# Optimization experiments

Hardware: AMD Instinct MI355X
Metric: run time of the kernel (lower is better)

The kernel has to match this reference:

```python
import jax, jax.numpy as jnp
import numpy as np

B, N, T, CIN, COUT, K, DIL = 8, 207, 12, 64, 64, 3, 1


def setup_inputs() -> dict:
    key = jax.random.key(0)
    ks = jax.random.split(key, 13)
    s = 0.05
    return {
        "X": jax.random.normal(ks[0], (B, N, T, CIN), jnp.float32),
        "wA": jax.random.normal(ks[1], (COUT, CIN, 1, K), jnp.float32) * s,
        "bA": jax.random.normal(ks[2], (COUT,), jnp.float32) * s,
        "wB": jax.random.normal(ks[3], (COUT, CIN, 1, K), jnp.float32) * s,
        "bB": jax.random.normal(ks[4], (COUT,), jnp.float32) * s,
        "wq": jax.random.normal(ks[5], (COUT // 8, COUT), jnp.float32) * s,
        "bq": jax.random.normal(ks[6], (COUT // 8,), jnp.float32) * s,
        "wk": jax.random.normal(ks[7], (COUT // 8, COUT), jnp.float32) * s,
        "bk": jax.random.normal(ks[8], (COUT // 8,), jnp.float32) * s,
        "wv": jax.random.normal(ks[9], (COUT, COUT), jnp.float32) * s,
        "bv": jax.random.normal(ks[10], (COUT,), jnp.float32) * s,
        "gamma": jax.random.normal(ks[11], (1,), jnp.float32) * 0.1,
    }


def reference(X, wA, bA, wB, bB, wq, bq, wk, bk, wv, bv, gamma):
    # X: [B, N, T, C] -> [B, C, N, T]
    x = jnp.transpose(X, (0, 3, 1, 2))
    k_size = wA.shape[-1]
    pad = (k_size - 1) * DIL  # causal left pad == pad-both + drop-right in torch code

    def causal_conv(w, b):
        y = jax.lax.conv_general_dilated(
            x, w, window_strides=(1, 1),
            padding=((0, 0), (pad, 0)),
            rhs_dilation=(1, DIL),
            dimension_numbers=("NCHW", "OIHW", "NCHW"))
        return y + b[None, :, None, None]

    A = causal_conv(wA, bA)
    Bg = causal_conv(wB, bB)
    h = A * jax.nn.sigmoid(Bg)  # [B, C, N, T]

    b_, c, w_, h_ = h.shape
    L = w_ * h_
    h2 = h.reshape(b_, c, L)  # [B, C, L]
    q = jnp.einsum("oc,bcl->bol", wq, h2) + bq[None, :, None]  # [B, C/8, L]
    kk = jnp.einsum("oc,bcl->bol", wk, h2) + bk[None, :, None]
    v = jnp.einsum("oc,bcl->bol", wv, h2) + bv[None, :, None]   # [B, C, L]

    energy = jnp.einsum("bql,bqm->blm", q, kk)  # [B, L, L]
    attn = jax.nn.softmax(energy, axis=-1)
    out = jnp.einsum("bcm,blm->bcl", v, attn).reshape(b_, c, w_, h_)
    out = gamma[0] * out + h
    return jnp.transpose(out, (0, 2, 3, 1))  # [B, N, T, C]
```

## Files before the change

### kernel.cpp

```cpp
#include <hip/hip_runtime.h>
#include <hip/hip_bf16.h>

#define Bn 8
#define Nn 207
#define Tn 12
#define Cn 64
#define Ln (Nn*Tn)
#define LP 2496
#define NT 39
#define NB 104

typedef unsigned int u32;
typedef unsigned short u16;
typedef _Float16 f16;
typedef __fp16 h16;
typedef __attribute__((ext_vector_type(2))) __fp16 h16x2;
typedef __attribute__((ext_vector_type(4))) __fp16 h16x4;
typedef __attribute__((ext_vector_type(4))) float floatx4;

#define LOG2E 1.44269504088896f

__device__ __forceinline__ u16 f2h(float f) { f16 h = (f16)f; return *(u16*)&h; }
__device__ __forceinline__ float h2f_lo(u32 u) { u16 x = (u16)u;        f16 h = *(f16*)&x; return (float)h; }
__device__ __forceinline__ float h2f_hi(u32 u) { u16 x = (u16)(u >> 16); f16 h = *(f16*)&x; return (float)h; }

#define W_PW   0
#define U_WVT  24576
#define F_WK   14336
#define F_WQ   14848
#define U_K    30720
#define U_Q    190464
#define U_HT   350208

__global__ __launch_bounds__(256) void prep_kernel(
    const float* __restrict__ wA, const float* __restrict__ wB,
    const float* __restrict__ wq, const float* __restrict__ wk,
    const float* __restrict__ wv, float* __restrict__ ws)
{
    u16* wsu = (u16*)ws;
    u32* wsw = (u32*)ws;
    int idx = blockIdx.x * 256 + threadIdx.x;
    if (idx < 12288) {
        int co = idx & 63, j = (idx >> 6) & 7, cig = (idx >> 9) & 7, k = idx >> 12;
        int src = (co*64 + cig*8 + j)*3 + k;
        wsw[W_PW + idx] = (u32)f2h(wA[src]) | ((u32)f2h(wB[src]) << 16);
    } else if (idx < 16384) {
        int j = idx - 12288;
        wsu[U_WVT + j] = f2h(wv[j]);
    } else if (idx < 16896) {
        int j = idx - 16384; int o = j & 7, c = j >> 3;
        ws[F_WK + j] = wk[o*Cn + c];
    } else if (idx < 17408) {
        int j = idx - 16896; int o = j & 7, c = j >> 3;
        ws[F_WQ + j] = wq[o*Cn + c] * LOG2E;
    } else if (idx < 18944) {
        int j = idx - 17408;
        int b = j / 192, rem = j - b*192;
        int which = rem / 96, rr = rem - which*96;
        wsu[(which ? U_Q : U_K) + (size_t)b*LP*8 + Ln*8 + rr] = 0;
    } else if (idx < 25088) {
        int j = idx - 18944;
        int b = j / 768, rem = j - b*768;
        int c = rem / 12, mm = 52 + (rem - c*12);
        int ss = mm >> 4, q = (mm >> 2) & 3, i = mm & 3;
        int cs = c >> 4, rm = c & 15;
        wsu[U_HT + (size_t)b*NT*4096 + ((38*16 + ss*4 + cs)*256 + (rm*4 + q)*4 + i)] = 0;
    }
}

__global__ __launch_bounds__(256, 2) void conv_k_kernel(
    const float* __restrict__ X,
    const float* __restrict__ bA, const float* __restrict__ bB,
    const float* __restrict__ bk, const float* __restrict__ bq,
    float* __restrict__ ws, float* __restrict__ out)
{
    __shared__ u32   w_s[12288];
    __shared__ float xs[Tn*Cn];
    __shared__ float hs[Tn*Cn];
    __shared__ float wkq_s[1024];
    int b = blockIdx.x & 7;
    int n = blockIdx.x >> 3;
    int tid = threadIdx.x;

    for (int i = tid; i < 3072; i += 256)
        ((uint4*)w_s)[i] = ((const uint4*)ws)[i];
    const float* Xp = X + (size_t)(b*Nn + n)*Tn*Cn;
    for (int i = tid; i < (Tn*Cn)/4; i += 256)
        ((float4*)xs)[i] = ((const float4*)Xp)[i];
    ((float4*)wkq_s)[tid] = ((const float4*)(ws + F_WK))[tid];
    __syncthreads();

    int co = tid & 63;
    int tg = tid >> 6;
    float aA[3] = {bA[co], bA[co], bA[co]};
    float aB[3] = {bB[co], bB[co], bB[co]};
    int tb = tg*3 - 2;

    #pragma unroll 1
    for (int cig = 0; cig < 8; ++cig) {
        float xr[5][8];
        #pragma unroll
        for (int d = 0; d < 5; ++d) {
            int tp = tb + d;
            if (tp >= 0) {
                float4 xa = *(const float4*)(xs + tp*Cn + cig*8);
                float4 xb = *(const float4*)(xs + tp*Cn + cig*8 + 4);
                xr[d][0]=xa.x; xr[d][1]=xa.y; xr[d][2]=xa.z; xr[d][3]=xa.w;
                xr[d][4]=xb.x; xr[d][5]=xb.y; xr[d][6]=xb.z; xr[d][7]=xb.w;
            } else {
                #pragma unroll
                for (int j = 0; j < 8; ++j) xr[d][j] = 0.f;
            }
        }
        #pragma unroll
        for (int k = 0; k < 3; ++k) {
            #pragma unroll
            for (int j = 0; j < 8; ++j) {
                u32 p = w_s[((k*8 + cig)*8 + j)*64 + co];
                float wa = h2f_lo(p), wb = h2f_hi(p);
                #pragma unroll
                for (int tt = 0; tt < 3; ++tt) {
                    aA[tt] += xr[tt + k][j] * wa;
                    aB[tt] += xr[tt + k][j] * wb;
                }
            }
        }
    }

    #pragma unroll
    for (int tt = 0; tt < 3; ++tt) {
        int t = tg*3 + tt;
        float hv = aA[tt] * (1.f / (1.f + __expf(-aB[tt])));
        hs[t*Cn + co] = hv;
        out[((size_t)b*Ln + (size_t)n*Tn + t)*Cn + co] = hv;
    }
    __syncthreads();

    if (tid < 96) {
        int r = tid >> 3, o = tid & 7;
        float acc = bk[o];
        for (int c = 0; c < Cn; ++c) acc += hs[r*Cn + c] * wkq_s[c*8 + o];
        ((u16*)ws)[U_K + (size_t)b*LP*8 + ((size_t)n*Tn + r)*8 + o] = f2h(acc);
    } else if (tid < 192) {
        int r = (tid - 96) >> 3, o = tid & 7;
        float acc = bq[o] * LOG2E;
        for (int c = 0; c < Cn; ++c) acc += hs[r*Cn + c] * wkq_s[512 + c*8 + o];
        ((u16*)ws)[U_Q + (size_t)b*LP*8 + ((size_t)n*Tn + r)*8 + o] = f2h(acc);
    }
    {
        int jj = tid >> 6, c = tid & 63;
        if (jj < 3) {
            int m = n*Tn + 4*jj;
            int tile = m >> 6, mloc = m & 63;
            int ss = mloc >> 4, q = (mloc >> 2) & 3;
            int cs = c >> 4, rm = c & 15;
            u32 p0 = ((u32)f2h(hs[(4*jj+1)*Cn + c]) << 16) | f2h(hs[(4*jj+0)*Cn + c]);
            u32 p1 = ((u32)f2h(hs[(4*jj+3)*Cn + c]) << 16) | f2h(hs[(4*jj+2)*Cn + c]);
            u16* ht = (u16*)ws + U_HT + (size_t)b*NT*4096
                    + ((tile*16 + ss*4 + cs)*256 + (rm*4 + q)*4);
            *(uint2*)ht = make_uint2(p0, p1);
        }
    }
}

__global__ __launch_bounds__(256, 3) void attn_kernel(
    const float* __restrict__ gamma, const float* __restrict__ bv,
    const float* __restrict__ ws, float* __restrict__ out)
{
    __shared__ float part[4*64*24];
    __shared__ float den_part[4][32];

    int b  = blockIdx.x & 7;
    int nb = blockIdx.x >> 3;
    int R0 = nb*24;
    int tid = threadIdx.x;
    int lane = tid & 63;
    int w = tid >> 6;
    int rm = lane & 15;
    int quad = lane >> 4;

    const u16* wsu = (const u16*)ws;
    const u16* kb = wsu + U_K  + (size_t)b*LP*8;
    const u16* qb = wsu + U_Q  + (size_t)b*LP*8;
    const u16* hb = wsu + U_HT + (size_t)b*NT*4096;

    h16x4 qf0, qf1;
    {
        uint2 u0 = make_uint2(0, 0), u1 = make_uint2(0, 0);
        int r0 = R0 + rm;       if (r0 >= LP) r0 = LP - 1;
        int r1 = R0 + 16 + rm;  if (r1 >= LP) r1 = LP - 1;
        if (quad < 2) {
            u0 = *(const uint2*)(qb + (size_t)r0*8 + 4*quad);
            u1 = *(const uint2*)(qb + (size_t)r1*8 + 4*quad);
        }
        qf0 = *(h16x4*)&u0; qf1 = *(h16x4*)&u1;
    }

    const h16x2 one2 = {(h16)1.f, (h16)1.f};

    floatx4 acc[4][2];
    #pragma unroll
    for (int cs = 0; cs < 4; ++cs)
        #pragma unroll
        for (int g = 0; g < 2; ++g) acc[cs][g] = (floatx4){0.f, 0.f, 0.f, 0.f};
    float dsum0 = 0.f, dsum1 = 0.f;

    uint2 k0_0,k0_1,k0_2,k0_3, k1_0,k1_1,k1_2,k1_3;
    uint2 h0_0,h0_1,h0_2,h0_3,h0_4,h0_5,h0_6,h0_7,h0_8,h0_9,h0_10,h0_11,h0_12,h0_13,h0_14,h0_15;
    uint2 h1_0,h1_1,h1_2,h1_3,h1_4,h1_5,h1_6,h1_7,h1_8,h1_9,h1_10,h1_11,h1_12,h1_13,h1_14,h1_15;

#define LDK(kt, SS) ((quad < 2) ? *(const uint2*)((kt) + ((SS)*16 + rm)*8 + 4*quad) : make_uint2(0,0))
#define LDH(ht, IDX) (*(const uint2*)((ht) + (IDX)*256 + lane*4))

#define LOADT(B, T) {                                                          \
    int tc = ((T) < NT) ? (T) : (NT-1);                                        \
    const u16* kt_ = kb + (size_t)tc*512;                                      \
    const u16* ht_ = hb + (size_t)tc*4096;                                     \
    k##B##_0 = LDK(kt_, 0); k##B##_1 = LDK(kt_, 1);                            \
    k##B##_2 = LDK(kt_, 2); k##B##_3 = LDK(kt_, 3);                            \
    h##B##_0  = LDH(ht_, 0);  h##B##_1  = LDH(ht_, 1);                         \
    h##B##_2  = LDH(ht_, 2);  h##B##_3  = LDH(ht_, 3);                         \
    h##B##_4  = LDH(ht_, 4);  h##B##_5  = LDH(ht_, 5);                         \
    h##B##_6  = LDH(ht_, 6);  h##B##_7  = LDH(ht_, 7);                         \
    h##B##_8  = LDH(ht_, 8);  h##B##_9  = LDH(ht_, 9);                         \
    h##B##_10 = LDH(ht_, 10); h##B##_11 = LDH(ht_, 11);                        \
    h##B##_12 = LDH(ht_, 12); h##B##_13 = LDH(ht_, 13);                        \
    h##B##_14 = LDH(ht_, 14); h##B##_15 = LDH(ht_, 15);                        \
}

#define COMPSS(KR, HA, HB_, HC, HD) {                                          \
    h16x4 kf = *(h16x4*)&KR;                                                   \
    floatx4 s0 = {0.f,0.f,0.f,0.f}, s1 = {0.f,0.f,0.f,0.f};                    \
    s0 = __builtin_amdgcn_mfma_f32_16x16x16f16(kf, qf0, s0, 0, 0, 0);          \
    s1 = __builtin_amdgcn_mfma_f32_16x16x16f16(kf, qf1, s1, 0, 0, 0);          \
    h16x2 e0a = __builtin_amdgcn_cvt_pkrtz(__builtin_amdgcn_exp2f(s0[0]),      \
                                           __builtin_amdgcn_exp2f(s0[1]));     \
    h16x2 e0b = __builtin_amdgcn_cvt_pkrtz(__builtin_amdgcn_exp2f(s0[2]),      \
                                           __builtin_amdgcn_exp2f(s0[3]));     \
    h16x2 e1a = __builtin_amdgcn_cvt_pkrtz(__builtin_amdgcn_exp2f(s1[0]),      \
                                           __builtin_amdgcn_exp2f(s1[1]));     \
    h16x2 e1b = __builtin_amdgcn_cvt_pkrtz(__builtin_amdgcn_exp2f(s1[2]),      \
                                           __builtin_amdgcn_exp2f(s1[3]));     \
    dsum0 = __builtin_amdgcn_fdot2(e0a, one2, dsum0, false);                   \
    dsum0 = __builtin_amdgcn_fdot2(e0b, one2, dsum0, false);                   \
    dsum1 = __builtin_amdgcn_fdot2(e1a, one2, dsum1, false);                   \
    dsum1 = __builtin_amdgcn_fdot2(e1b, one2, dsum1, false);                   \
    h16x4 e0 = __builtin_shufflevector(e0a, e0b, 0, 1, 2, 3);                  \
    h16x4 e1 = __builtin_shufflevector(e1a, e1b, 0, 1, 2, 3);                  \
    h16x4 a0_ = *(h16x4*)&HA, a1_ = *(h16x4*)&HB_, a2_ = *(h16x4*)&HC, a3_ = *(h16x4*)&HD; \
    acc[0][0] = __builtin_amdgcn_mfma_f32_16x16x16f16(a0_, e0, acc[0][0], 0, 0, 0); \
    acc[0][1] = __builtin_amdgcn_mfma_f32_16x16x16f16(a0_, e1, acc[0][1], 0, 0, 0); \
    acc[1][0] = __builtin_amdgcn_mfma_f32_16x16x16f16(a1_, e0, acc[1][0], 0, 0, 0); \
    acc[1][1] = __builtin_amdgcn_mfma_f32_16x16x16f16(a1_, e1, acc[1][1], 0, 0, 0); \
    acc[2][0] = __builtin_amdgcn_mfma_f32_16x16x16f16(a2_, e0, acc[2][0], 0, 0, 0); \
    acc[2][1] = __builtin_amdgcn_mfma_f32_16x16x16f16(a2_, e1, acc[2][1], 0, 0, 0); \
    acc[3][0] = __builtin_amdgcn_mfma_f32_16x16x16f16(a3_, e0, acc[3][0], 0, 0, 0); \
    acc[3][1] = __builtin_amdgcn_mfma_f32_16x16x16f16(a3_, e1, acc[3][1], 0, 0, 0); \
}

#define COMPT(B) {                                                             \
    COMPSS(k##B##_0, h##B##_0,  h##B##_1,  h##B##_2,  h##B##_3)                \
    COMPSS(k##B##_1, h##B##_4,  h##B##_5,  h##B##_6,  h##B##_7)                \
    COMPSS(k##B##_2, h##B##_8,  h##B##_9,  h##B##_10, h##B##_11)               \
    COMPSS(k##B##_3, h##B##_12, h##B##_13, h##B##_14, h##B##_15)               \
}

    LOADT(0, w)
    for (int i = 0; i < 4; ++i) {
        int t0 = w + 8*i;
        LOADT(1, t0 + 4)
        COMPT(0)
        LOADT(0, t0 + 8)
        COMPT(1)
    }
    if (w < 3) LOADT(1, w + 36)
    COMPT(0)
    if (w < 3) COMPT(1)
#undef LOADT
#undef COMPT
#undef COMPSS
#undef LDK
#undef LDH

    {
        float s_ = dsum0;
        s_ += __shfl_xor(s_, 16, 64);
        s_ += __shfl_xor(s_, 32, 64);
        if (quad == 0) den_part[w][rm] = s_;
        float t_ = dsum1;
        t_ += __shfl_xor(t_, 16, 64);
        t_ += __shfl_xor(t_, 32, 64);
        if (quad == 0) den_part[w][16 + rm] = t_;
    }

    float* pw = part + w*1536;
    #pragma unroll
    for (int cs = 0; cs < 4; ++cs) {
        #pragma unroll
        for (int i = 0; i < 4; ++i)
            pw[(cs*16 + quad*4 + i)*24 + rm] = acc[cs][0][i];
        if (rm < 8) {
            #pragma unroll
            for (int i = 0; i < 4; ++i)
                pw[(cs*16 + quad*4 + i)*24 + 16 + rm] = acc[cs][1][i];
        }
    }
    __syncthreads();

    for (int j = tid; j < 1536; j += 256)
        part[j] = part[j] + part[1536 + j] + part[3072 + j] + part[4608 + j];
    __syncthreads();

    int o = tid & 63, rq = tid >> 6;
    float gam = gamma[0];
    float bvo = bv[o];
    const u16* wvr = wsu + U_WVT + o*64;
    uint4 wvu[8];
    #pragma unroll
    for (int x = 0; x < 8; ++x) wvu[x] = *(const uint4*)(wvr + x*8);
    #pragma unroll
    for (int rr = 0; rr < 6; ++rr) {
        int r = rq*6 + rr;
        int row = R0 + r;
        if (row < Ln) {
            float den = den_part[0][r] + den_part[1][r] + den_part[2][r] + den_part[3][r]
                      - 12.0f;
            float p = 0.f;
            #pragma unroll
            for (int x = 0; x < 8; ++x) {
                const f16* hh = (const f16*)&wvu[x];
                #pragma unroll
                for (int i = 0; i < 8; ++i)
                    p += (float)hh[i] * part[(x*8 + i)*24 + r];
            }
            size_t gi = ((size_t)b*Ln + row)*64 + o;
            out[gi] = gam*(bvo + p/den) + out[gi];
        }
    }
}

extern "C" void kernel_launch(void* const* d_in, const int* in_sizes, int n_in,
                              void* d_out, int out_size, void* d_ws, size_t ws_size,
                              hipStream_t stream) {
    const float* X     = (const float*)d_in[0];
    const float* wA    = (const float*)d_in[1];
    const float* bA    = (const float*)d_in[2];
    const float* wB    = (const float*)d_in[3];
    const float* bB    = (const float*)d_in[4];
    const float* wq    = (const float*)d_in[5];
    const float* bq    = (const float*)d_in[6];
    const float* wk    = (const float*)d_in[7];
    const float* bk    = (const float*)d_in[8];
    const float* wv    = (const float*)d_in[9];
    const float* bv    = (const float*)d_in[10];
    const float* gamma = (const float*)d_in[11];
    float* out = (float*)d_out;
    float* ws  = (float*)d_ws;

    prep_kernel<<<98, 256, 0, stream>>>(wA, wB, wq, wk, wv, ws);
    conv_k_kernel<<<Bn*Nn, 256, 0, stream>>>(X, bA, bB, bk, bq, ws, out);
    attn_kernel<<<Bn*NB, 256, 0, stream>>>(gamma, bv, ws, out);
}
```

Baseline: 153.5 us.

## Keep conv weights in registers, split input channels, loop over nodes persistently

The conv kernel stops copying the 48KB packed weight table into shared memory for every block. Each warp-group now holds its slice of the weights (two input-channel groups) in registers and computes all 12 timesteps. Partial sums from the four groups are reduced through shared memory. The grid shrinks to 832 persistent blocks, each looping over about two nodes, and the k/q projection uses a rotated channel index to avoid LDS bank conflicts. This removes the repeated weight loads at the cost of more registers, an extra reduction pass and extra barriers.

Result: slower. 422.9 us (+175.5%).

```diff
diff --git a/kernel.cpp b/kernel.cpp
--- a/kernel.cpp
+++ b/kernel.cpp
@@ -68,97 +68,121 @@
     }
 }
 
-__global__ __launch_bounds__(256, 2) void conv_k_kernel(
+__global__ __launch_bounds__(256, 4) void conv_k_kernel(
     const float* __restrict__ X,
     const float* __restrict__ bA, const float* __restrict__ bB,
     const float* __restrict__ bk, const float* __restrict__ bq,
     float* __restrict__ ws, float* __restrict__ out)
 {
-    __shared__ u32   w_s[12288];
     __shared__ float xs[Tn*Cn];
+    __shared__ float red[4*Tn*Cn*2];
     __shared__ float hs[Tn*Cn];
     __shared__ float wkq_s[1024];
-    int b = blockIdx.x & 7;
-    int n = blockIdx.x >> 3;
     int tid = threadIdx.x;
-
-    for (int i = tid; i < 3072; i += 256)
-        ((uint4*)w_s)[i] = ((const uint4*)ws)[i];
-    const float* Xp = X + (size_t)(b*Nn + n)*Tn*Cn;
-    for (int i = tid; i < (Tn*Cn)/4; i += 256)
-        ((float4*)xs)[i] = ((const float4*)Xp)[i];
+    int co  = tid & 63;
+    int g   = tid >> 6;
+
     ((float4*)wkq_s)[tid] = ((const float4*)(ws + F_WK))[tid];
-    __syncthreads();
-
-    int co = tid & 63;
-    int tg = tid >> 6;
-    float aA[3] = {bA[co], bA[co], bA[co]};
-    float aB[3] = {bB[co], bB[co], bB[co]};
-    int tb = tg*3 - 2;
-
-    #pragma unroll 1
-    for (int cig = 0; cig < 8; ++cig) {
-        float xr[5][8];
-        #pragma unroll
-        for (int d = 0; d < 5; ++d) {
-            int tp = tb + d;
-            if (tp >= 0) {
-                float4 xa = *(const float4*)(xs + tp*Cn + cig*8);
-                float4 xb = *(const float4*)(xs + tp*Cn + cig*8 + 4);
-                xr[d][0]=xa.x; xr[d][1]=xa.y; xr[d][2]=xa.z; xr[d][3]=xa.w;
-                xr[d][4]=xb.x; xr[d][5]=xb.y; xr[d][6]=xb.z; xr[d][7]=xb.w;
-            } else {
+
+    const u32* wsw = (const u32*)ws;
+    u32 wreg[2][3][8];
+    #pragma unroll
+    for (int cc = 0; cc < 2; ++cc)
+        #pragma unroll
+        for (int k = 0; k < 3; ++k)
+            #pragma unroll
+            for (int j = 0; j < 8; ++j)
+                wreg[cc][k][j] = wsw[W_PW + ((k*8 + (2*g + cc))*8 + j)*64 + co];
+
+    float bAv = bA[co], bBv = bB[co];
+    int o_ = tid & 7;
+    float bko = 0.f;
+    if (tid < 96) bko = bk[o_];
+    else if (tid < 192) bko = bq[o_] * LOG2E;
+
+    int b  = blockIdx.x & 7;
+    int n0 = blockIdx.x >> 3;
+    u16* wsu16 = (u16*)ws;
+
+    for (int n = n0; n < Nn; n += 104) {
+        if (tid < 192)
+            ((float4*)xs)[tid] = ((const float4*)(X + (size_t)(b*Nn + n)*Tn*Cn))[tid];
+        __syncthreads();
+
+        float aA[12], aB[12];
+        #pragma unroll
+        for (int t = 0; t < 12; ++t) { aA[t] = 0.f; aB[t] = 0.f; }
+
+        #pragma unroll
+        for (int cc = 0; cc < 2; ++cc) {
+            int cbase = (2*g + cc)*8;
+            #pragma unroll
+            for (int j = 0; j < 8; ++j) {
+                float xv[12];
                 #pragma unroll
-                for (int j = 0; j < 8; ++j) xr[d][j] = 0.f;
-            }
-        }
-        #pragma unroll
-        for (int k = 0; k < 3; ++k) {
-            #pragma unroll
-            for (int j = 0; j < 8; ++j) {
-                u32 p = w_s[((k*8 + cig)*8 + j)*64 + co];
-                float wa = h2f_lo(p), wb = h2f_hi(p);
+                for (int t = 0; t < 12; ++t) xv[t] = xs[t*Cn + cbase + j];
                 #pragma unroll
-                for (int tt = 0; tt < 3; ++tt) {
-                    aA[tt] += xr[tt + k][j] * wa;
-                    aB[tt] += xr[tt + k][j] * wb;
+                for (int k = 0; k < 3; ++k) {
+                    u32 p = wreg[cc][k][j];
+                    float wa = h2f_lo(p), wb = h2f_hi(p);
+                    #pragma unroll
+                    for (int tp = 0; tp < 12; ++tp) {
+                        int t = tp + 2 - k;
+                        if (t < 12) { aA[t] += xv[tp]*wa; aB[t] += xv[tp]*wb; }
+                    }
                 }
             }
         }
-    }
-
-    #pragma unroll
-    for (int tt = 0; tt < 3; ++tt) {
-        int t = tg*3 + tt;
-        float hv = aA[tt] * (1.f / (1.f + __expf(-aB[tt])));
-        hs[t*Cn + co] = hv;
-        out[((size_t)b*Ln + (size_t)n*Tn + t)*Cn + co] = hv;
-    }
-    __syncthreads();
-
-    if (tid < 96) {
-        int r = tid >> 3, o = tid & 7;
-        float acc = bk[o];
-        for (int c = 0; c < Cn; ++c) acc += hs[r*Cn + c] * wkq_s[c*8 + o];
-        ((u16*)ws)[U_K + (size_t)b*LP*8 + ((size_t)n*Tn + r)*8 + o] = f2h(acc);
-    } else if (tid < 192) {
-        int r = (tid - 96) >> 3, o = tid & 7;
-        float acc = bq[o] * LOG2E;
-        for (int c = 0; c < Cn; ++c) acc += hs[r*Cn + c] * wkq_s[512 + c*8 + o];
-        ((u16*)ws)[U_Q + (size_t)b*LP*8 + ((size_t)n*Tn + r)*8 + o] = f2h(acc);
-    }
-    {
-        int jj = tid >> 6, c = tid & 63;
-        if (jj < 3) {
-            int m = n*Tn + 4*jj;
-            int tile = m >> 6, mloc = m & 63;
-            int ss = mloc >> 4, q = (mloc >> 2) & 3;
-            int cs = c >> 4, rm = c & 15;
-            u32 p0 = ((u32)f2h(hs[(4*jj+1)*Cn + c]) << 16) | f2h(hs[(4*jj+0)*Cn + c]);
-            u32 p1 = ((u32)f2h(hs[(4*jj+3)*Cn + c]) << 16) | f2h(hs[(4*jj+2)*Cn + c]);
-            u16* ht = (u16*)ws + U_HT + (size_t)b*NT*4096
-                    + ((tile*16 + ss*4 + cs)*256 + (rm*4 + q)*4);
-            *(uint2*)ht = make_uint2(p0, p1);
+        #pragma unroll
+        for (int t = 0; t < 12; ++t)
+            *(float2*)&red[(((g*12 + t)*64) + co)*2] = float2{aA[t], aB[t]};
+        __syncthreads();
+
+        #pragma unroll
+        for (int tt = 0; tt < 3; ++tt) {
+            int t = g*3 + tt;
+            float sA = bAv, sB = bBv;
+            #pragma unroll
+            for (int gg = 0; gg < 4; ++gg) {
+                float2 f2 = *(const float2*)&red[(((gg*12 + t)*64) + co)*2];
+                sA += f2.x; sB += f2.y;
+            }
+            float hv = sA * (1.f / (1.f + __expf(-sB)));
+            hs[t*Cn + co] = hv;
+            out[((size_t)b*Ln + (size_t)n*Tn + t)*Cn + co] = hv;
+        }
+        __syncthreads();
+
+        if (tid < 96) {
+            int r = tid >> 3;
+            float acc = bko;
+            for (int ci = 0; ci < Cn; ++ci) {
+                int c = (ci + r) & 63;
+                acc += hs[r*Cn + c] * wkq_s[c*8 + o_];
+            }
+            wsu16[U_K + (size_t)b*LP*8 + ((size_t)n*Tn + r)*8 + o_] = f2h(acc);
+        } else if (tid < 192) {
+            int r = (tid - 96) >> 3;
+            float acc = bko;
+            for (int ci = 0; ci < Cn; ++ci) {
+                int c = (ci + r) & 63;
+                acc += hs[r*Cn + c] * wkq_s[512 + c*8 + o_];
+            }
+            wsu16[U_Q + (size_t)b*LP*8 + ((size_t)n*Tn + r)*8 + o_] = f2h(acc);
+        }
+        {
+            int jj = tid >> 6, c = tid & 63;
+            if (jj < 3) {
+                int m = n*Tn + 4*jj;
+                int tile = m >> 6, mloc = m & 63;
+                int ss = mloc >> 4, q = (mloc >> 2) & 3;
+                int cs = c >> 4, rm = c & 15;
+                u32 p0 = ((u32)f2h(hs[(4*jj+1)*Cn + c]) << 16) | f2h(hs[(4*jj+0)*Cn + c]);
+                u32 p1 = ((u32)f2h(hs[(4*jj+3)*Cn + c]) << 16) | f2h(hs[(4*jj+2)*Cn + c]);
+                u16* ht = wsu16 + U_HT + (size_t)b*NT*4096
+                        + ((tile*16 + ss*4 + cs)*256 + (rm*4 + q)*4);
+                *(uint2*)ht = make_uint2(p0, p1);
+            }
         }
     }
 }
@@ -358,6 +382,6 @@
     float* ws  = (float*)d_ws;
 
     prep_kernel<<<98, 256, 0, stream>>>(wA, wB, wq, wk, wv, ws);
-    conv_k_kernel<<<Bn*Nn, 256, 0, stream>>>(X, bA, bB, bk, bq, ws, out);
+    conv_k_kernel<<<Bn*NB, 256, 0, stream>>>(X, bA, bB, bk, bq, ws, out);
     attn_kernel<<<Bn*NB, 256, 0, stream>>>(gamma, bv, ws, out);
 }
```
